# Performance work log

Measured on AMD Instinct MI355X. Metric: run time of the kernel, lower is better.

## Reference

```python
import jax, jax.numpy as jnp
import numpy as np
import math

B, S, D = 4, 2048, 1024      # batch, seq, d_model
E, F_EXP = 16, 512           # n_experts_ffn, d_expert_ffn
N_SHARED, K_FFN = 2, 4       # shared experts, routed top-k
N_ROUTED = E - N_SHARED


def setup_inputs() -> dict:
    key = jax.random.key(0)
    k0, k1, k2, k3, k4 = jax.random.split(key, 5)
    token_stream = jax.random.normal(k0, (B, S, D), jnp.float32)
    selection_input = jax.random.normal(k1, (B, S, D), jnp.float32)
    # init per reset_parameters (std_scale = 1.0)
    keys_w = jax.random.normal(k2, (E, D, F_EXP), jnp.float32) / math.sqrt(D)
    values_w = jax.random.normal(k3, (E, F_EXP, D), jnp.float32) / math.sqrt(E * F_EXP)
    expert_sel = jax.random.normal(k4, (E, D), jnp.float32) / math.sqrt(D)
    bias_ffn = jnp.zeros((E,), jnp.float32)  # load-balancing bias buffer
    return {
        "token_stream": token_stream,
        "selection_input": selection_input,
        "keys_w": keys_w,
        "values_w": values_w,
        "expert_sel": expert_sel,
        "bias_ffn": bias_ffn,
    }


def reference(token_stream, selection_input, keys_w, values_w, expert_sel, bias_ffn):
    # ---- routing: sigmoid affinity over all experts ----
    affinity = jax.nn.sigmoid(jnp.einsum("bsd,ed->bse", selection_input, expert_sel))  # [B,S,E]
    # top-k over routed experts (bias only affects ranking, not gathered affinity)
    _, routed_idx = jax.lax.top_k(affinity[..., :N_ROUTED] + bias_ffn[:N_ROUTED], K_FFN)  # [B,S,k]
    shared_idx = jnp.broadcast_to(
        jnp.arange(N_ROUTED, E, dtype=routed_idx.dtype), routed_idx.shape[:-1] + (N_SHARED,)
    )
    sel = jnp.concatenate([routed_idx, shared_idx], axis=-1)  # [B,S,K], K = k + shared
    aff_sel = jnp.take_along_axis(affinity, sel, axis=-1)     # [B,S,K]

    # ---- expert FFN (cvmm = gather / grouped GEMM / weighted scatter) ----
    # dense per-expert key projection, then gather selected experts
    scores_all = jnp.einsum("bsd,edf->bsef", token_stream, keys_w)        # [B,S,E,f]
    scores = jnp.take_along_axis(scores_all, sel[..., None], axis=2)      # [B,S,K,f]
    scores = jax.nn.silu(scores)

    # combine: out = sum_k aff_k * (scores_k @ values[sel_k])
    onehot = jax.nn.one_hot(sel, E, dtype=scores.dtype)                   # [B,S,K,E]
    dispatch = jnp.einsum("bskf,bske->bsef", scores * aff_sel[..., None], onehot)  # [B,S,E,f]
    out = jnp.einsum("bsef,efd->bsd", dispatch, values_w)                 # [B,S,D]
    return out, sel
```

## Files before the change

### kernel.cpp

```cpp
#include <hip/hip_runtime.h>

typedef short short8 __attribute__((ext_vector_type(8)));
typedef float f32x4 __attribute__((ext_vector_type(4)));
typedef unsigned short u16;

#define TOK_N 8192
#define DMODEL 1024
#define NEXP 16
#define FEXP 512
#define NROUTED 14
#define KSEL 6

__device__ __forceinline__ u16 f2bf(float f) {
  unsigned u = __float_as_uint(f);
  u += 0x7fff + ((u >> 16) & 1);
  return (u16)(u >> 16);
}

typedef const __attribute__((address_space(1))) unsigned int* gas_p;
typedef __attribute__((address_space(3))) unsigned int* las_p;
__device__ __forceinline__ void gload_lds16(const void* g, void* l) {
  __builtin_amdgcn_global_load_lds((gas_p)g, (las_p)l, 16, 0, 0);
}

__global__ void cast_bf16_k(const float* __restrict__ in, u16* __restrict__ out, int n8) {
  int i = blockIdx.x * blockDim.x + threadIdx.x;
  if (i >= n8) return;
  const float4* p = (const float4*)(in + (size_t)i * 8);
  float4 a = p[0], b = p[1];
  short8 v;
  v[0] = (short)f2bf(a.x); v[1] = (short)f2bf(a.y); v[2] = (short)f2bf(a.z); v[3] = (short)f2bf(a.w);
  v[4] = (short)f2bf(b.x); v[5] = (short)f2bf(b.y); v[6] = (short)f2bf(b.z); v[7] = (short)f2bf(b.w);
  *(short8*)(out + (size_t)i * 8) = v;
}

__global__ void transpose_cast_k(const float* __restrict__ in, u16* __restrict__ out, int R, int C) {
  __shared__ u16 tile[32][33];
  int e = blockIdx.z;
  int c0 = blockIdx.x * 32, r0 = blockIdx.y * 32;
  int x = threadIdx.x, y = threadIdx.y;
  const float* ip = in + ((size_t)e * R + r0) * C + c0;
  #pragma unroll
  for (int i = 0; i < 4; i++)
    tile[y + 8 * i][x] = f2bf(ip[(size_t)(y + 8 * i) * C + x]);
  __syncthreads();
  u16* op = out + ((size_t)e * C + c0) * R + r0;
  #pragma unroll
  for (int i = 0; i < 4; i++)
    op[(size_t)(y + 8 * i) * R + x] = tile[x][y + 8 * i];
}

__global__ void routing_k(const float* __restrict__ selin, const float* __restrict__ esel,
                          const float* __restrict__ bias, float* __restrict__ out_sel,
                          unsigned* __restrict__ sel_pack, float* __restrict__ aff6) {
  int tok = blockIdx.x;
  int t = threadIdx.x;
  int e = t & 15, chunk = t >> 4;
  const float4* r4 = (const float4*)(selin + (size_t)tok * DMODEL + chunk * 64);
  const float4* w4 = (const float4*)(esel + (size_t)e * DMODEL + chunk * 64);
  float p = 0.f;
  #pragma unroll
  for (int i = 0; i < 16; i++) {
    float4 a = r4[i], b = w4[i];
    p += a.x * b.x + a.y * b.y + a.z * b.z + a.w * b.w;
  }
  __shared__ float part[16][17];
  __shared__ float aff[16];
  __shared__ float lbias[NROUTED];
  if (t < NROUTED) lbias[t] = bias[t];
  part[chunk][e] = p;
  __syncthreads();
  if (t < 16) {
    float s = 0.f;
    #pragma unroll
    for (int c = 0; c < 16; c++) s += part[c][t];
    aff[t] = 1.f / (1.f + expf(-s));
  }
  __syncthreads();
  if (t == 0) {
    unsigned pack = 0;
    unsigned taken = 0;
    #pragma unroll
    for (int k = 0; k < 4; k++) {
      float best = -3.4e38f; int bi = 0;
      for (int q = 0; q < NROUTED; q++) {
        if (taken & (1u << q)) continue;
        float v = aff[q] + lbias[q];
        if (v > best) { best = v; bi = q; }
      }
      taken |= 1u << bi;
      pack |= (unsigned)bi << (4 * k);
      out_sel[(size_t)tok * KSEL + k] = (float)bi;
      aff6[(size_t)tok * KSEL + k] = aff[bi];
    }
    pack |= 14u << 16; pack |= 15u << 20;
    out_sel[(size_t)tok * KSEL + 4] = 14.f;
    out_sel[(size_t)tok * KSEL + 5] = 15.f;
    aff6[(size_t)tok * KSEL + 4] = aff[14];
    aff6[(size_t)tok * KSEL + 5] = aff[15];
    sel_pack[tok] = pack;
  }
}

__global__ void scatter_k(const unsigned* __restrict__ sel_pack, const float* __restrict__ aff6,
                          int* __restrict__ counts, int* __restrict__ tokk,
                          float* __restrict__ affl) {
  __shared__ int lcnt[16], lbase[16], lcur[16];
  int t = threadIdx.x;
  int tok = blockIdx.x * 256 + t;
  if (t < 16) lcnt[t] = 0;
  __syncthreads();
  unsigned pack = sel_pack[tok];
  int eid[KSEL];
  #pragma unroll
  for (int k = 0; k < KSEL; k++) {
    eid[k] = (pack >> (4 * k)) & 15;
    atomicAdd(&lcnt[eid[k]], 1);
  }
  __syncthreads();
  if (t < 16) {
    lbase[t] = atomicAdd(&counts[t * 16], lcnt[t]);
    lcur[t] = 0;
  }
  __syncthreads();
  #pragma unroll
  for (int k = 0; k < KSEL; k++) {
    int e = eid[k];
    int slot = lbase[e] + atomicAdd(&lcur[e], 1);
    tokk[e * TOK_N + slot] = tok * 8 + k;
    affl[e * TOK_N + slot] = aff6[(size_t)tok * KSEL + k];
  }
}

template<int AK, int PASS>
__global__ __launch_bounds__(256) void moe_gemm_k(
    const u16* __restrict__ Abase, const u16* __restrict__ Bbase,
    const int* __restrict__ counts, const int* __restrict__ tokk,
    const float* __restrict__ affl, u16* __restrict__ scores_out,
    float* __restrict__ out) {
  int e = blockIdx.z;
  int cnt = counts[e * 16];
  int m0 = blockIdx.x * 128;
  if (m0 >= cnt) return;
  int n0 = blockIdx.y * 128;
  int t = threadIdx.x;
  int lane = t & 63, w = t >> 6;
  int wr = w >> 1, wc = w & 1;

  __shared__ u16 Al[128][64];
  __shared__ u16 Bl[128][64];

  const int* tl = tokk + e * TOK_N + m0;
  const float* al = affl + e * TOK_N + m0;
  const u16* Bp = Bbase + (size_t)e * 524288;

  f32x4 acc[4][4];
  #pragma unroll
  for (int m = 0; m < 4; m++)
    #pragma unroll
    for (int n = 0; n < 4; n++)
      acc[m][n] = (f32x4){0.f, 0.f, 0.f, 0.f};

  int jj = lane & 7, rl = lane >> 3;
  const u16* ag[4]; const u16* bg[4];
  #pragma unroll
  for (int r = 0; r < 4; r++) {
    int row = r * 32 + w * 8 + rl;
    int lr = (m0 + row < cnt) ? row : 0;
    int tk = tl[lr];
    int ar = (PASS == 2) ? (tk >> 3) : ((tk >> 3) * 6 + (tk & 7));
    int cs = (jj ^ (row & 7)) * 8;
    ag[r] = Abase + (size_t)ar * AK + cs;
    bg[r] = Bp + (size_t)(n0 + row) * AK + cs;
  }

  for (int k0 = 0; k0 < AK; k0 += 64) {
    #pragma unroll
    for (int r = 0; r < 4; r++) {
      gload_lds16(ag[r] + k0, &Al[r * 32 + w * 8][0]);
      gload_lds16(bg[r] + k0, &Bl[r * 32 + w * 8][0]);
    }
    __syncthreads();
    #pragma unroll
    for (int kk = 0; kk < 2; kk++) {
      int lc = kk * 4 + (lane >> 4);
      short8 af[4], bf[4];
      #pragma unroll
      for (int m = 0; m < 4; m++) {
        int row = wr * 64 + m * 16 + (lane & 15);
        af[m] = *(const short8*)&Al[row][(lc ^ (row & 7)) * 8];
      }
      #pragma unroll
      for (int n = 0; n < 4; n++) {
        int row = wc * 64 + n * 16 + (lane & 15);
        bf[n] = *(const short8*)&Bl[row][(lc ^ (row & 7)) * 8];
      }
      #pragma unroll
      for (int m = 0; m < 4; m++)
        #pragma unroll
        for (int n = 0; n < 4; n++)
          acc[m][n] = __builtin_amdgcn_mfma_f32_16x16x32_bf16(af[m], bf[n], acc[m][n], 0, 0, 0);
    }
    __syncthreads();
  }

  int cbase = n0 + wc * 64 + (lane & 15);
  #pragma unroll
  for (int m = 0; m < 4; m++) {
    int rbase = wr * 64 + m * 16 + ((lane >> 4) << 2);
    #pragma unroll
    for (int q = 0; q < 4; q++) {
      int row = rbase + q;
      if (m0 + row >= cnt) continue;
      int tk = tl[row];
      if (PASS == 2) {
        float aff = al[row];
        size_t base = (size_t)((tk >> 3) * 6 + (tk & 7)) * FEXP;
        #pragma unroll
        for (int n = 0; n < 4; n++) {
          float v = acc[m][n][q];
          float s = aff * v / (1.f + expf(-v));
          scores_out[base + cbase + n * 16] = f2bf(s);
        }
      } else {
        size_t base = (size_t)(tk >> 3) * DMODEL;
        #pragma unroll
        for (int n = 0; n < 4; n++)
          atomicAdd(&out[base + cbase + n * 16], acc[m][n][q]);
      }
    }
  }
}

extern "C" void kernel_launch(void* const* d_in, const int* in_sizes, int n_in,
                              void* d_out, int out_size, void* d_ws, size_t ws_size,
                              hipStream_t stream) {
  (void)in_sizes; (void)n_in; (void)out_size; (void)ws_size;
  const float* token_stream    = (const float*)d_in[0];
  const float* selection_input = (const float*)d_in[1];
  const float* keys_w          = (const float*)d_in[2];
  const float* values_w        = (const float*)d_in[3];
  const float* expert_sel      = (const float*)d_in[4];
  const float* bias_ffn        = (const float*)d_in[5];

  float* out     = (float*)d_out;
  float* out_sel = out + (size_t)TOK_N * DMODEL;

  char* ws = (char*)d_ws;
  u16*      Xbf      = (u16*)(ws + 0);
  u16*      keysT    = (u16*)(ws + 16777216);
  u16*      valuesT  = (u16*)(ws + 33554432);
  u16*      scoresbf = (u16*)(ws + 50331648);
  int*      counts   = (int*)(ws + 100663296);
  int*      tokk     = (int*)(ws + 100664320);
  float*    affl     = (float*)(ws + 101188608);
  unsigned* sel_pack = (unsigned*)(ws + 101712896);
  float*    aff6     = (float*)(ws + 101745664);

  hipMemsetAsync(out, 0, (size_t)TOK_N * DMODEL * sizeof(float), stream);
  hipMemsetAsync(counts, 0, 1024, stream);

  cast_bf16_k<<<4096, 256, 0, stream>>>(token_stream, Xbf, TOK_N * DMODEL / 8);
  transpose_cast_k<<<dim3(16, 32, 16), dim3(32, 8), 0, stream>>>(keys_w, keysT, 1024, 512);
  transpose_cast_k<<<dim3(32, 16, 16), dim3(32, 8), 0, stream>>>(values_w, valuesT, 512, 1024);

  routing_k<<<TOK_N, 256, 0, stream>>>(selection_input, expert_sel, bias_ffn,
                                       out_sel, sel_pack, aff6);
  scatter_k<<<TOK_N / 256, 256, 0, stream>>>(sel_pack, aff6, counts, tokk, affl);

  moe_gemm_k<1024, 2><<<dim3(64, 4, 16), 256, 0, stream>>>(Xbf, keysT, counts, tokk, affl,
                                                           scoresbf, nullptr);
  moe_gemm_k<512, 3><<<dim3(64, 8, 16), 256, 0, stream>>>(scoresbf, valuesT, counts, tokk, affl,
                                                          nullptr, out);
}
```

Before: 461.4 us.

## Compact MoE GEMM grid with device-built tile list and raise occupancy hint

```diff
diff --git a/kernel.cpp b/kernel.cpp
--- a/kernel.cpp
+++ b/kernel.cpp
@@ -10,6 +10,7 @@
 #define FEXP 512
 #define NROUTED 14
 #define KSEL 6
+#define MAXTILES 400
 
 __device__ __forceinline__ u16 f2bf(float f) {
   unsigned u = __float_as_uint(f);
@@ -132,16 +133,31 @@
   }
 }
 
+__global__ void tilelist_k(const int* __restrict__ counts, int* __restrict__ tiles,
+                           int* __restrict__ ntiles) {
+  if (threadIdx.x != 0 || blockIdx.x != 0) return;
+  int tcnt[16];
+  for (int e = 0; e < 16; e++) tcnt[e] = (counts[e * 16] + 127) >> 7;
+  int n = 0;
+  for (int i = 0; i < 64; i++)
+    for (int e = 0; e < 16; e++)
+      if (i < tcnt[e]) tiles[n++] = e | (i << 8);
+  *ntiles = n;
+}
+
 template<int AK, int PASS>
-__global__ __launch_bounds__(256) void moe_gemm_k(
+__global__ __launch_bounds__(256, 4) void moe_gemm_k(
     const u16* __restrict__ Abase, const u16* __restrict__ Bbase,
     const int* __restrict__ counts, const int* __restrict__ tokk,
-    const float* __restrict__ affl, u16* __restrict__ scores_out,
+    const float* __restrict__ affl, const int* __restrict__ tiles,
+    const int* __restrict__ ntiles, u16* __restrict__ scores_out,
     float* __restrict__ out) {
-  int e = blockIdx.z;
+  int slot = blockIdx.x;
+  if (slot >= *ntiles) return;
+  int desc = tiles[slot];
+  int e = desc & 15;
+  int m0 = (desc >> 8) << 7;
   int cnt = counts[e * 16];
-  int m0 = blockIdx.x * 128;
-  if (m0 >= cnt) return;
   int n0 = blockIdx.y * 128;
   int t = threadIdx.x;
   int lane = t & 63, w = t >> 6;
@@ -256,6 +272,8 @@
   float*    affl     = (float*)(ws + 101188608);
   unsigned* sel_pack = (unsigned*)(ws + 101712896);
   float*    aff6     = (float*)(ws + 101745664);
+  int*      tiles    = (int*)(ws + 101942272);
+  int*      ntiles   = (int*)(ws + 101946368);
 
   hipMemsetAsync(out, 0, (size_t)TOK_N * DMODEL * sizeof(float), stream);
   hipMemsetAsync(counts, 0, 1024, stream);
@@ -267,9 +285,10 @@
   routing_k<<<TOK_N, 256, 0, stream>>>(selection_input, expert_sel, bias_ffn,
                                        out_sel, sel_pack, aff6);
   scatter_k<<<TOK_N / 256, 256, 0, stream>>>(sel_pack, aff6, counts, tokk, affl);
-
-  moe_gemm_k<1024, 2><<<dim3(64, 4, 16), 256, 0, stream>>>(Xbf, keysT, counts, tokk, affl,
-                                                           scoresbf, nullptr);
-  moe_gemm_k<512, 3><<<dim3(64, 8, 16), 256, 0, stream>>>(scoresbf, valuesT, counts, tokk, affl,
-                                                          nullptr, out);
-}
+  tilelist_k<<<1, 64, 0, stream>>>(counts, tiles, ntiles);
+
+  moe_gemm_k<1024, 2><<<dim3(MAXTILES, 4), 256, 0, stream>>>(Xbf, keysT, counts, tokk, affl,
+                                                             tiles, ntiles, scoresbf, nullptr);
+  moe_gemm_k<512, 3><<<dim3(MAXTILES, 8), 256, 0, stream>>>(scoresbf, valuesT, counts, tokk, affl,
+                                                            tiles, ntiles, nullptr, out);
+}
```

Result: slower. 486.7 us (+5.5%).
